# Kernel tuning notes

Hardware: AMD Instinct MI355X
Metric: run time of the kernel (lower is better)

The kernel has to match this reference:

```python
import jax, jax.numpy as jnp
import numpy as np

B, D, H, W = 16, 64, 64, 64
K = 1024


def setup_inputs() -> dict:
    key = jax.random.key(0)
    k1, k2 = jax.random.split(key)
    x = jax.random.normal(k1, (B, D, H, W), dtype=jnp.float32)
    limit = 3.0 ** 0.5
    e_i_ts = jax.random.uniform(k2, (D, K), dtype=jnp.float32, minval=-limit, maxval=limit)
    return {"x": x, "e_i_ts": e_i_ts}


def reference(x, e_i_ts):
    b, d, h, w = x.shape
    # [B,H,W,D] -> [N,D]
    flat_x = jnp.transpose(x, (0, 2, 3, 1)).reshape(-1, d)
    distances = (
        jnp.sum(flat_x * flat_x, axis=1, keepdims=True)
        - 2.0 * (flat_x @ e_i_ts)
        + jnp.sum(e_i_ts * e_i_ts, axis=0, keepdims=True)
    )
    encoding_indices = jnp.argmin(distances, axis=1)  # [N]
    reshaped_indices = encoding_indices.reshape(b, h, w)
    # codebook gather: e_i_ts.T is [K,D]
    quantized = jnp.take(e_i_ts.T, reshaped_indices, axis=0)  # [B,H,W,D]
    quantized_x = jnp.transpose(quantized, (0, 3, 1, 2))  # [B,D,H,W]

    dictionary_loss = jnp.mean((jax.lax.stop_gradient(x) - quantized_x) ** 2)
    commitment_loss = jnp.mean((x - jax.lax.stop_gradient(quantized_x)) ** 2)
    # straight-through estimator
    quantized_x = x + jax.lax.stop_gradient(quantized_x - x)
    return quantized_x, dictionary_loss, commitment_loss, encoding_indices.reshape(b, -1)
```

## Files before the change

### kernel.cpp

```cpp
#include <hip/hip_runtime.h>

#define DD 64
#define KK 1024
#define NPTS 65536
#define TOTAL 4194304

#define OFF_L1 4194304
#define OFF_L2 4194305
#define OFF_IDX 4194306

#define WS_ENH_F 64
#define WS_EHT_BYTE 65536
#define WS_ELT_BYTE (65536 + 131072)

#define MARGIN_S 0.006f

typedef __attribute__((ext_vector_type(8))) short short8;
typedef __attribute__((ext_vector_type(4))) float f32x4;

__device__ __forceinline__ unsigned short bf16_rne(float f) {
    unsigned b = __float_as_uint(f);
    return (unsigned short)((b + 0x7FFFu + ((b >> 16) & 1u)) >> 16);
}
__device__ __forceinline__ float bf16_to_f(unsigned short h) {
    return __uint_as_float(((unsigned)h) << 16);
}
__device__ __forceinline__ unsigned umax(unsigned a, unsigned b) { return a > b ? a : b; }
__device__ __forceinline__ unsigned umin(unsigned a, unsigned b) { return a < b ? a : b; }
__device__ __forceinline__ void gld_lds16(const void* g, void* l) {
    __builtin_amdgcn_global_load_lds(
        (const __attribute__((address_space(1))) void*)g,
        (__attribute__((address_space(3))) void*)l, 16, 0, 0);
}
__device__ __forceinline__ int swz(int r, int d) {
    return ((d & ~7) ^ ((r & 7) << 3)) | (d & 7);
}

__global__ __launch_bounds__(256) void prep_kernel(const float* __restrict__ e,
                                                   float* __restrict__ enh,
                                                   unsigned short* __restrict__ ehT,
                                                   unsigned short* __restrict__ elT,
                                                   float* __restrict__ sum,
                                                   unsigned* __restrict__ tick) {
    const int tid = threadIdx.x;
    if (blockIdx.x == 0 && tid == 0) { *sum = 0.f; *tick = 0u; }
    const int wave = tid >> 6, lane = tid & 63;
    const int k = blockIdx.x * 4 + wave;
    const float v = e[lane * KK + k];
    const unsigned short h = bf16_rne(v);
    const unsigned short l = bf16_rne(v - bf16_to_f(h));
    const int pos = k * 64 + swz(k, lane);
    ehT[pos] = h;
    elT[pos] = l;
    float s2 = v * v;
#pragma unroll
    for (int m = 32; m > 0; m >>= 1) s2 += __shfl_down(s2, m, 64);
    if (lane == 0) enh[k] = 512.0f - 0.5f * s2;
}

__global__ __launch_bounds__(256, 5) void vq_gemm(const float* __restrict__ x,
                                                  const float* __restrict__ e,
                                                  const float* __restrict__ enh,
                                                  const unsigned short* __restrict__ ehT,
                                                  const unsigned short* __restrict__ elT,
                                                  float* __restrict__ out,
                                                  float* __restrict__ sum,
                                                  unsigned* __restrict__ tick) {
    __shared__ __align__(16) char ebuf[2 * 16384];

    float* mv1 = (float*)ebuf;
    float* mv2 = mv1 + 128;
    int*   mi1 = (int*)(mv2 + 128);
    int*   ks  = mi1 + 128;
    float* xnp = (float*)(ks + 64);
    float* lv  = xnp + 64;
    float* xp  = lv + 64;
    int*   rl  = (int*)(xp + 64);
    int*   rn  = rl + 64;
    float* rv  = (float*)(rn + 1);
    int*   ri  = (int*)(rv + 4);

    const int tid = threadIdx.x;
    const int wave = tid >> 6, lane = tid & 63;
    const int n0 = blockIdx.x * 64;
    const int b = n0 >> 12;
    const int hw0 = n0 & 4095;

    const char* ehTb = (const char*)ehT;
    const char* elTb = (const char*)elT;
    const int lofs = wave * 1024 + lane * 16;

    {
        char* db = ebuf;
        gld_lds16(ehTb + lofs,        db + wave * 1024);
        gld_lds16(ehTb + 4096 + lofs, db + 4096 + wave * 1024);
        gld_lds16(elTb + lofs,        db + 8192 + wave * 1024);
        gld_lds16(elTb + 4096 + lofs, db + 12288 + wave * 1024);
    }

    float* xsc = (float*)(ebuf + 16384);
    {
        const int d = tid >> 2, ph = tid & 3;
        const float* src = x + ((b * DD + d) << 12) + hw0 + ph * 16;
        float* dst = xsc + d * 64 + ph * 16;
#pragma unroll
        for (int j = 0; j < 4; ++j)
            *(float4*)(dst + j * 4) = *(const float4*)(src + j * 4);
    }
    __syncthreads();
    const int p = tid >> 2, dq = tid & 3;
    float xv[16];
    float xn = 0.f;
#pragma unroll
    for (int s = 0; s < 16; ++s) {
        xv[s] = xsc[(dq * 16 + s) * 64 + p];
        xn = fmaf(xv[s], xv[s], xn);
    }
    xn += __shfl_down(xn, 1, 64);
    xn += __shfl_down(xn, 2, 64);
    __syncthreads();
    unsigned short* xbh = (unsigned short*)(ebuf + 16384);
    unsigned short* xbl = (unsigned short*)(ebuf + 16384 + 8192);
    {
#pragma unroll
        for (int g = 0; g < 2; ++g) {
            short8 hh, ll;
#pragma unroll
            for (int j = 0; j < 8; ++j) {
                const float f = xv[g * 8 + j];
                const unsigned short h = bf16_rne(f);
                hh[j] = (short)h;
                ll[j] = (short)bf16_rne(f - bf16_to_f(h));
            }
            const int pos = p * 64 + ((dq * 16 + g * 8) ^ ((p & 7) << 3));
            *(short8*)(xbh + pos) = hh;
            *(short8*)(xbl + pos) = ll;
        }
    }
    __syncthreads();

    const int ln15 = lane & 15, q8 = (lane >> 4) * 8;
    const int wp = (wave >> 1) * 32;
    const int wc = (wave & 1) * 32;

    short8 ah[2][2], al[2][2];
#pragma unroll
    for (int rf = 0; rf < 2; ++rf)
#pragma unroll
        for (int kc = 0; kc < 2; ++kc) {
            const int pp = wp + rf * 16 + ln15;
            const int pos = pp * 64 + ((kc * 32 + q8) ^ ((pp & 7) << 3));
            ah[rf][kc] = *(const short8*)(xbh + pos);
            al[rf][kc] = *(const short8*)(xbl + pos);
        }

    unsigned v1u[8], v2u[8];
#pragma unroll
    for (int r = 0; r < 8; ++r) { v1u[r] = 0u; v2u[r] = 0u; }

    for (int kt = 0; kt < 16; ++kt) {
        __syncthreads();
        if (kt < 15) {
            const int nkt = kt + 1;
            char* db = ebuf + (nkt & 1) * 16384;
            const char* sH = ehTb + nkt * 8192 + lofs;
            const char* sL = elTb + nkt * 8192 + lofs;
            gld_lds16(sH,        db + wave * 1024);
            gld_lds16(sH + 4096, db + 4096 + wave * 1024);
            gld_lds16(sL,        db + 8192 + wave * 1024);
            gld_lds16(sL + 4096, db + 12288 + wave * 1024);
        }
        const unsigned short* ebH = (const unsigned short*)(ebuf + (kt & 1) * 16384);
        const unsigned short* ebL = ebH + 4096;

        f32x4 acc[2][2];
#pragma unroll
        for (int cf = 0; cf < 2; ++cf) {
            const float ec = enh[kt * 64 + wc + cf * 16 + ln15];
#pragma unroll
            for (int rf = 0; rf < 2; ++rf)
                acc[rf][cf] = (f32x4){ec, ec, ec, ec};
        }

#pragma unroll
        for (int kc = 0; kc < 2; ++kc) {
            short8 bh[2], bl[2];
#pragma unroll
            for (int cf = 0; cf < 2; ++cf) {
                const int c = wc + cf * 16 + ln15;
                const int pos = c * 64 + ((kc * 32 + q8) ^ ((c & 7) << 3));
                bh[cf] = *(const short8*)(ebH + pos);
                bl[cf] = *(const short8*)(ebL + pos);
            }
#pragma unroll
            for (int rf = 0; rf < 2; ++rf)
#pragma unroll
                for (int cf = 0; cf < 2; ++cf) {
                    acc[rf][cf] = __builtin_amdgcn_mfma_f32_16x16x32_bf16(al[rf][kc], bh[cf], acc[rf][cf], 0, 0, 0);
                    acc[rf][cf] = __builtin_amdgcn_mfma_f32_16x16x32_bf16(ah[rf][kc], bl[cf], acc[rf][cf], 0, 0, 0);
                    acc[rf][cf] = __builtin_amdgcn_mfma_f32_16x16x32_bf16(ah[rf][kc], bh[cf], acc[rf][cf], 0, 0, 0);
                }
        }

#pragma unroll
        for (int rf = 0; rf < 2; ++rf)
#pragma unroll
            for (int reg = 0; reg < 4; ++reg) {
                const int r = rf * 4 + reg;
                const unsigned k0 = (__float_as_uint(acc[rf][0][reg]) | 31u) ^ (unsigned)(kt * 2 + 0);
                const unsigned k1 = (__float_as_uint(acc[rf][1][reg]) | 31u) ^ (unsigned)(kt * 2 + 1);
                const unsigned a = umax(k0, k1), bb = umin(k0, k1);
                v2u[r] = umax(umax(v2u[r], umin(v1u[r], a)), bb);
                v1u[r] = umax(v1u[r], a);
            }
    }

    if ((tid & 3) == 0) xnp[p] = xn;
    if (tid == 0) *rn = 0;

#pragma unroll
    for (int r = 0; r < 8; ++r) {
        const unsigned c5 = 31u - (v1u[r] & 31u);
        int col = (int)(c5 >> 1) * 64 + wc + (int)(c5 & 1) * 16 + ln15;
        float val = __uint_as_float(v1u[r] & ~31u);
        float sec = __uint_as_float(v2u[r] & ~31u);
#pragma unroll
        for (int msk = 1; msk < 16; msk <<= 1) {
            const float ov = __shfl_xor(val, msk);
            const int oc = __shfl_xor(col, msk);
            const float os = __shfl_xor(sec, msk);
            sec = fmaxf(fmaxf(sec, os), fminf(val, ov));
            const bool t = (ov > val) || (ov == val && oc < col);
            val = t ? ov : val;
            col = t ? oc : col;
        }
        if (ln15 == 0) {
            const int q = lane >> 4;
            const int h = wave & 1;
            const int pt = wp + (r >> 2) * 16 + q * 4 + (r & 3);
            mv1[pt * 2 + h] = val;
            mi1[pt * 2 + h] = col;
            mv2[pt * 2 + h] = sec;
        }
    }
    __syncthreads();
    if (tid < 64) {
        const float va = mv1[tid * 2], vb = mv1[tid * 2 + 1];
        const int ia = mi1[tid * 2], ib = mi1[tid * 2 + 1];
        const bool t = (vb > va) || (vb == va && ib < ia);
        const float bv = t ? vb : va;
        const int bi = t ? ib : ia;
        const float sec = fmaxf(fmaxf(mv2[tid * 2], mv2[tid * 2 + 1]), fminf(va, vb));
        ks[tid] = bi;
        lv[tid] = xnp[tid] + 1024.0f - 2.0f * bv;
        if (bv - sec < MARGIN_S) {
            const int w = atomicAdd(rn, 1);
            rl[w] = tid;
        }
    }
    __syncthreads();

    const int lcnt = *rn;
    for (int it = 0; it < lcnt; ++it) {
        const int pr = rl[it];
        if (tid < 64) xp[tid] = x[((b * DD + tid) << 12) + hw0 + pr];
        __syncthreads();
        float d0 = 0.f, d1 = 0.f, d2 = 0.f, d3 = 0.f;
#pragma unroll 8
        for (int dd = 0; dd < DD; ++dd) {
            const float xd = xp[dd];
            const float4 ev = *(const float4*)(e + dd * KK + tid * 4);
            d0 = fmaf(xd, ev.x, d0);
            d1 = fmaf(xd, ev.y, d1);
            d2 = fmaf(xd, ev.z, d2);
            d3 = fmaf(xd, ev.w, d3);
        }
        const float4 ea = *(const float4*)(enh + tid * 4);
        float bs = d0 + ea.x;
        int bi2 = tid * 4;
        if (d1 + ea.y > bs) { bs = d1 + ea.y; bi2 = tid * 4 + 1; }
        if (d2 + ea.z > bs) { bs = d2 + ea.z; bi2 = tid * 4 + 2; }
        if (d3 + ea.w > bs) { bs = d3 + ea.w; bi2 = tid * 4 + 3; }
#pragma unroll
        for (int m = 1; m < 64; m <<= 1) {
            const float ov = __shfl_xor(bs, m, 64);
            const int oi = __shfl_xor(bi2, m, 64);
            if (ov > bs || (ov == bs && oi < bi2)) { bs = ov; bi2 = oi; }
        }
        if (lane == 0) { rv[wave] = bs; ri[wave] = bi2; }
        __syncthreads();
        if (tid == 0) {
            float gs = rv[0];
            int gi = ri[0];
#pragma unroll
            for (int t2 = 1; t2 < 4; ++t2)
                if (rv[t2] > gs || (rv[t2] == gs && ri[t2] < gi)) { gs = rv[t2]; gi = ri[t2]; }
            ks[pr] = gi;
            lv[pr] = xnp[pr] + 1024.0f - 2.0f * gs;
        }
        __syncthreads();
    }

    if (tid < 64) {
        out[OFF_IDX + n0 + tid] = (float)ks[tid];
        float lc = lv[tid];
#pragma unroll
        for (int off = 32; off > 0; off >>= 1) lc += __shfl_down(lc, off, 64);
        if (tid == 0) {
            atomicAdd(sum, lc);
            __threadfence();
            const unsigned old = atomicAdd(tick, 1u);
            if (old == (unsigned)(gridDim.x - 1)) {
                const float s = atomicAdd(sum, 0.0f);
                const float m = s * (1.0f / (float)TOTAL);
                out[OFF_L1] = m;
                out[OFF_L2] = m;
            }
        }
    }

    {
        const int pe = tid & 63, dqr = tid >> 6;
        const int kp = ks[pe];
        const int kx = (kp & 7) << 3;
        float qa[16];
#pragma unroll
        for (int g = 0; g < 2; ++g) {
            const int pos = kp * 64 + ((dqr * 16 + g * 8) ^ kx);
            const short8 h8 = *(const short8*)(ehT + pos);
            const short8 l8 = *(const short8*)(elT + pos);
#pragma unroll
            for (int j = 0; j < 8; ++j)
                qa[g * 8 + j] = bf16_to_f((unsigned short)h8[j]) + bf16_to_f((unsigned short)l8[j]);
        }
        float* ob = out + ((b * DD + dqr * 16) << 12) + hw0 + pe;
#pragma unroll
        for (int s = 0; s < 16; ++s) ob[s << 12] = qa[s];
    }
}

extern "C" void kernel_launch(void* const* d_in, const int* in_sizes, int n_in,
                              void* d_out, int out_size, void* d_ws, size_t ws_size,
                              hipStream_t stream) {
    const float* x = (const float*)d_in[0];
    const float* e = (const float*)d_in[1];
    float* out = (float*)d_out;

    float* sum = (float*)d_ws;
    unsigned* tick = (unsigned*)d_ws + 2;
    float* enh = (float*)d_ws + WS_ENH_F;
    unsigned short* ehT = (unsigned short*)((char*)d_ws + WS_EHT_BYTE);
    unsigned short* elT = (unsigned short*)((char*)d_ws + WS_ELT_BYTE);

    prep_kernel<<<256, 256, 0, stream>>>(e, enh, ehT, elT, sum, tick);
    vq_gemm<<<NPTS / 64, 256, 0, stream>>>(x, e, enh, ehT, elT, out, sum, tick);
}
```

Baseline: 140.6 us.

## Restructure prep transpose via LDS, compute loss directly, gather from fp32 codebook

The prep kernel now runs 16 blocks that each load 64 codewords coalesced, convert them to hi/lo bf16, transpose through shared memory and write out contiguous swizzled tiles. The main kernel drops the per-point x-norm path and computes the loss directly as the sum of (x - q)^2 while re-reading x and gathering the fp32 codebook during the output write. Shared memory becomes separate static arrays, the bf16 split of x is written element by element, and the occupancy hint of 5 is removed from launch bounds. This trades the algebraic loss shortcut for an extra read of x, and changes LDS footprint and occupancy.

```diff
diff --git a/kernel.cpp b/kernel.cpp
--- a/kernel.cpp
+++ b/kernel.cpp
@@ -42,43 +42,69 @@
                                                    unsigned short* __restrict__ elT,
                                                    float* __restrict__ sum,
                                                    unsigned* __restrict__ tick) {
-    const int tid = threadIdx.x;
+    __shared__ unsigned short tH[64 * 64];
+    __shared__ unsigned short tL[64 * 64];
+    __shared__ float ps[4 * 64];
+    const int tid = threadIdx.x, wave = tid >> 6, lane = tid & 63;
     if (blockIdx.x == 0 && tid == 0) { *sum = 0.f; *tick = 0u; }
-    const int wave = tid >> 6, lane = tid & 63;
-    const int k = blockIdx.x * 4 + wave;
-    const float v = e[lane * KK + k];
-    const unsigned short h = bf16_rne(v);
-    const unsigned short l = bf16_rne(v - bf16_to_f(h));
-    const int pos = k * 64 + swz(k, lane);
-    ehT[pos] = h;
-    elT[pos] = l;
-    float s2 = v * v;
-#pragma unroll
-    for (int m = 32; m > 0; m >>= 1) s2 += __shfl_down(s2, m, 64);
-    if (lane == 0) enh[k] = 512.0f - 0.5f * s2;
-}
-
-__global__ __launch_bounds__(256, 5) void vq_gemm(const float* __restrict__ x,
-                                                  const float* __restrict__ e,
-                                                  const float* __restrict__ enh,
-                                                  const unsigned short* __restrict__ ehT,
-                                                  const unsigned short* __restrict__ elT,
-                                                  float* __restrict__ out,
-                                                  float* __restrict__ sum,
-                                                  unsigned* __restrict__ tick) {
+    const int k = blockIdx.x * 64 + lane;
+    float s2 = 0.f;
+    short8 hh[2], ll[2];
+#pragma unroll
+    for (int g = 0; g < 2; ++g)
+#pragma unroll
+        for (int j = 0; j < 8; ++j) {
+            const int d = wave * 16 + g * 8 + j;
+            const float v = e[d * KK + k];
+            const unsigned short h = bf16_rne(v);
+            hh[g][j] = (short)h;
+            ll[g][j] = (short)bf16_rne(v - bf16_to_f(h));
+            s2 = fmaf(v, v, s2);
+        }
+    ps[wave * 64 + lane] = s2;
+#pragma unroll
+    for (int g = 0; g < 2; ++g) {
+        const int pos = lane * 64 + ((wave * 16 + g * 8) ^ ((k & 7) << 3));
+        *(short8*)(tH + pos) = hh[g];
+        *(short8*)(tL + pos) = ll[g];
+    }
+    __syncthreads();
+    if (wave == 0) {
+        const float t = ps[lane] + ps[64 + lane] + ps[128 + lane] + ps[192 + lane];
+        enh[k] = 512.0f - 0.5f * t;
+    }
+    {
+        const short8* srcH = (const short8*)tH;
+        const short8* srcL = (const short8*)tL;
+        short8* dstH = (short8*)(ehT + blockIdx.x * 64 * 64);
+        short8* dstL = (short8*)(elT + blockIdx.x * 64 * 64);
+        dstH[tid * 2]     = srcH[tid * 2];
+        dstH[tid * 2 + 1] = srcH[tid * 2 + 1];
+        dstL[tid * 2]     = srcL[tid * 2];
+        dstL[tid * 2 + 1] = srcL[tid * 2 + 1];
+    }
+}
+
+__global__ __launch_bounds__(256) void vq_gemm(const float* __restrict__ x,
+                                               const float* __restrict__ e,
+                                               const float* __restrict__ enh,
+                                               const unsigned short* __restrict__ ehT,
+                                               const unsigned short* __restrict__ elT,
+                                               float* __restrict__ out,
+                                               float* __restrict__ sum,
+                                               unsigned* __restrict__ tick) {
     __shared__ __align__(16) char ebuf[2 * 16384];
-
-    float* mv1 = (float*)ebuf;
-    float* mv2 = mv1 + 128;
-    int*   mi1 = (int*)(mv2 + 128);
-    int*   ks  = mi1 + 128;
-    float* xnp = (float*)(ks + 64);
-    float* lv  = xnp + 64;
-    float* xp  = lv + 64;
-    int*   rl  = (int*)(xp + 64);
-    int*   rn  = rl + 64;
-    float* rv  = (float*)(rn + 1);
-    int*   ri  = (int*)(rv + 4);
+    __shared__ __align__(16) unsigned short xbh[64 * 64];
+    __shared__ __align__(16) unsigned short xbl[64 * 64];
+    __shared__ float mv1[64 * 2], mv2[64 * 2];
+    __shared__ int mi1[64 * 2];
+    __shared__ int ks[64];
+    __shared__ float red[4];
+    __shared__ float xp[64];
+    __shared__ int rl[64];
+    __shared__ int rn;
+    __shared__ float rv[4];
+    __shared__ int ri[4];
 
     const int tid = threadIdx.x;
     const int wave = tid >> 6, lane = tid & 63;
@@ -97,6 +123,7 @@
         gld_lds16(elTb + lofs,        db + 8192 + wave * 1024);
         gld_lds16(elTb + 4096 + lofs, db + 12288 + wave * 1024);
     }
+    if (tid == 0) rn = 0;
 
     float* xsc = (float*)(ebuf + 16384);
     {
@@ -108,33 +135,16 @@
             *(float4*)(dst + j * 4) = *(const float4*)(src + j * 4);
     }
     __syncthreads();
-    const int p = tid >> 2, dq = tid & 3;
-    float xv[16];
-    float xn = 0.f;
-#pragma unroll
-    for (int s = 0; s < 16; ++s) {
-        xv[s] = xsc[(dq * 16 + s) * 64 + p];
-        xn = fmaf(xv[s], xv[s], xn);
-    }
-    xn += __shfl_down(xn, 1, 64);
-    xn += __shfl_down(xn, 2, 64);
-    __syncthreads();
-    unsigned short* xbh = (unsigned short*)(ebuf + 16384);
-    unsigned short* xbl = (unsigned short*)(ebuf + 16384 + 8192);
     {
-#pragma unroll
-        for (int g = 0; g < 2; ++g) {
-            short8 hh, ll;
-#pragma unroll
-            for (int j = 0; j < 8; ++j) {
-                const float f = xv[g * 8 + j];
-                const unsigned short h = bf16_rne(f);
-                hh[j] = (short)h;
-                ll[j] = (short)bf16_rne(f - bf16_to_f(h));
-            }
-            const int pos = p * 64 + ((dq * 16 + g * 8) ^ ((p & 7) << 3));
-            *(short8*)(xbh + pos) = hh;
-            *(short8*)(xbl + pos) = ll;
+        const int p = tid >> 2, dq = tid & 3;
+#pragma unroll
+        for (int s = 0; s < 16; ++s) {
+            const int d = dq * 16 + s;
+            const float f = xsc[d * 64 + p];
+            const unsigned short h = bf16_rne(f);
+            const int pos = p * 64 + swz(p, d);
+            xbh[pos] = h;
+            xbl[pos] = bf16_rne(f - bf16_to_f(h));
         }
     }
     __syncthreads();
@@ -215,9 +225,6 @@
             }
     }
 
-    if ((tid & 3) == 0) xnp[p] = xn;
-    if (tid == 0) *rn = 0;
-
 #pragma unroll
     for (int r = 0; r < 8; ++r) {
         const unsigned c5 = 31u - (v1u[r] & 31u);
@@ -252,15 +259,14 @@
         const int bi = t ? ib : ia;
         const float sec = fmaxf(fmaxf(mv2[tid * 2], mv2[tid * 2 + 1]), fminf(va, vb));
         ks[tid] = bi;
-        lv[tid] = xnp[tid] + 1024.0f - 2.0f * bv;
         if (bv - sec < MARGIN_S) {
-            const int w = atomicAdd(rn, 1);
+            const int w = atomicAdd(&rn, 1);
             rl[w] = tid;
         }
     }
     __syncthreads();
 
-    const int lcnt = *rn;
+    const int lcnt = rn;
     for (int it = 0; it < lcnt; ++it) {
         const int pr = rl[it];
         if (tid < 64) xp[tid] = x[((b * DD + tid) << 12) + hw0 + pr];
@@ -296,46 +302,38 @@
             for (int t2 = 1; t2 < 4; ++t2)
                 if (rv[t2] > gs || (rv[t2] == gs && ri[t2] < gi)) { gs = rv[t2]; gi = ri[t2]; }
             ks[pr] = gi;
-            lv[pr] = xnp[pr] + 1024.0f - 2.0f * gs;
         }
         __syncthreads();
     }
 
-    if (tid < 64) {
-        out[OFF_IDX + n0 + tid] = (float)ks[tid];
-        float lc = lv[tid];
-#pragma unroll
-        for (int off = 32; off > 0; off >>= 1) lc += __shfl_down(lc, off, 64);
-        if (tid == 0) {
-            atomicAdd(sum, lc);
-            __threadfence();
-            const unsigned old = atomicAdd(tick, 1u);
-            if (old == (unsigned)(gridDim.x - 1)) {
-                const float s = atomicAdd(sum, 0.0f);
-                const float m = s * (1.0f / (float)TOTAL);
-                out[OFF_L1] = m;
-                out[OFF_L2] = m;
-            }
-        }
-    }
-
-    {
-        const int pe = tid & 63, dqr = tid >> 6;
-        const int kp = ks[pe];
-        const int kx = (kp & 7) << 3;
-        float qa[16];
-#pragma unroll
-        for (int g = 0; g < 2; ++g) {
-            const int pos = kp * 64 + ((dqr * 16 + g * 8) ^ kx);
-            const short8 h8 = *(const short8*)(ehT + pos);
-            const short8 l8 = *(const short8*)(elT + pos);
-#pragma unroll
-            for (int j = 0; j < 8; ++j)
-                qa[g * 8 + j] = bf16_to_f((unsigned short)h8[j]) + bf16_to_f((unsigned short)l8[j]);
-        }
-        float* ob = out + ((b * DD + dqr * 16) << 12) + hw0 + pe;
-#pragma unroll
-        for (int s = 0; s < 16; ++s) ob[s << 12] = qa[s];
+    if (tid < 64) out[OFF_IDX + n0 + tid] = (float)ks[tid];
+
+    const int p = tid & 63, dqr = tid >> 6;
+    const int kp = ks[p];
+    float lacc = 0.f;
+#pragma unroll
+    for (int s = 0; s < 16; ++s) {
+        const int d = dqr * 16 + s;
+        const float qv = e[d * KK + kp];
+        const float xv = x[((b * DD + d) << 12) + hw0 + p];
+        out[((b * DD + d) << 12) + hw0 + p] = qv;
+        const float df = xv - qv;
+        lacc = fmaf(df, df, lacc);
+    }
+#pragma unroll
+    for (int off = 32; off > 0; off >>= 1) lacc += __shfl_down(lacc, off, 64);
+    if (lane == 0) red[wave] = lacc;
+    __syncthreads();
+    if (tid == 0) {
+        atomicAdd(sum, red[0] + red[1] + red[2] + red[3]);
+        __threadfence();
+        const unsigned old = atomicAdd(tick, 1u);
+        if (old == (unsigned)(gridDim.x - 1)) {
+            const float s = atomicAdd(sum, 0.0f);
+            const float m = s * (1.0f / (float)TOTAL);
+            out[OFF_L1] = m;
+            out[OFF_L2] = m;
+        }
     }
 }
 
@@ -352,6 +350,6 @@
     unsigned short* ehT = (unsigned short*)((char*)d_ws + WS_EHT_BYTE);
     unsigned short* elT = (unsigned short*)((char*)d_ws + WS_ELT_BYTE);
 
-    prep_kernel<<<256, 256, 0, stream>>>(e, enh, ehT, elT, sum, tick);
+    prep_kernel<<<KK / 64, 256, 0, stream>>>(e, enh, ehT, elT, sum, tick);
     vq_gemm<<<NPTS / 64, 256, 0, stream>>>(x, e, enh, ehT, elT, out, sum, tick);
 }
```

Result: slower. 145.5 us (+3.5%).
